# Optimization experiments

Hardware: AMD Instinct MI355X
Metric: run time of the kernel (lower is better)

## Reference

```python
import jax, jax.numpy as jnp
import numpy as np

C = 256
INTER = 32  # C // reduction_ratio(8)
B, H, W = 4, 64, 64


def setup_inputs() -> dict:
    key = jax.random.key(0)
    ks = jax.random.split(key, 8)
    x = jax.random.normal(ks[0], (B, C, H, W), dtype=jnp.float32)
    # 1x1 conv weights stored as [out, in] matrices + biases
    Wq = jax.random.normal(ks[1], (INTER, C), dtype=jnp.float32) * (1.0 / np.sqrt(C))
    bq = jnp.zeros((INTER,), dtype=jnp.float32)
    Wk = jax.random.normal(ks[2], (INTER, C), dtype=jnp.float32) * (1.0 / np.sqrt(C))
    bk = jnp.zeros((INTER,), dtype=jnp.float32)
    Wv = jax.random.normal(ks[3], (C, C), dtype=jnp.float32) * (1.0 / np.sqrt(C))
    bv = jnp.zeros((C,), dtype=jnp.float32)
    gamma = jnp.zeros((1,), dtype=jnp.float32)
    return {"x": x, "Wq": Wq, "bq": bq, "Wk": Wk, "bk": bk, "Wv": Wv, "bv": bv, "gamma": gamma}


def reference(x, Wq, bq, Wk, bk, Wv, bv, gamma):
    b, c, h, w = x.shape
    n = h * w
    xf = x.reshape(b, c, n)  # [B,C,N]
    # 1x1 convs == channel matmuls
    q = jnp.einsum('ic,bcn->bin', Wq, xf) + bq[None, :, None]  # [B,I,N]
    k = jnp.einsum('ic,bcn->bin', Wk, xf) + bk[None, :, None]  # [B,I,N]
    v = jnp.einsum('oc,bcn->bon', Wv, xf) + bv[None, :, None]  # [B,C,N]
    scale = INTER ** (-0.5)
    attn = jnp.einsum('bin,bim->bnm', q, k) * scale  # [B,N,N]
    attn = jax.nn.softmax(attn, axis=-1)
    out = jnp.einsum('bcm,bnm->bcn', v, attn)  # value @ attn^T
    out = out.reshape(b, c, h, w)
    return gamma[0] * out + x
```

## Files before the change

kernel.cpp:

```cpp
#include <hip/hip_runtime.h>
#include <hip/hip_bf16.h>
#include <cstddef>
#include <cstdint>

#define BB 4
#define CC 256
#define II 32
#define NN 4096

#define SCALE_Q 0.25505572751402893f

typedef __attribute__((ext_vector_type(8))) short bf16x8;
typedef __attribute__((ext_vector_type(16))) float f32x16;

static __device__ __forceinline__ int cvt_pk_bf16(float lo, float hi) {
  int d;
  asm("v_cvt_pk_bf16_f32 %0, %1, %2" : "=v"(d) : "v"(lo), "v"(hi));
  return d;
}
static __device__ __forceinline__ void perm32swap_i(int& a, int& b) {
  asm("v_permlane32_swap_b32 %0, %1" : "+v"(a), "+v"(b));
}
static __device__ __forceinline__ void perm32swap_f(float& a, float& b) {
  asm("v_permlane32_swap_b32 %0, %1" : "+v"(a), "+v"(b));
}
static __device__ __forceinline__ float max3f(float a, float b, float c) {
  float d;
  asm("v_max3_f32 %0, %1, %2, %3" : "=v"(d) : "v"(a), "v"(b), "v"(c));
  return d;
}
static __device__ __forceinline__ f32x16 zero16() {
  f32x16 z;
#pragma unroll
  for (int i = 0; i < 16; ++i) z[i] = 0.0f;
  return z;
}
static __device__ __forceinline__ bf16x8 pack8(float f0, float f1, float f2,
    float f3, float f4, float f5, float f6, float f7) {
  union { int w[4]; bf16x8 v8; } u;
  u.w[0] = cvt_pk_bf16(f0, f1);
  u.w[1] = cvt_pk_bf16(f2, f3);
  u.w[2] = cvt_pk_bf16(f4, f5);
  u.w[3] = cvt_pk_bf16(f6, f7);
  return u.v8;
}
static __device__ __forceinline__ ushort f2bfu(float f) {
  union { __hip_bfloat16 h; ushort u; } cv;
  cv.h = __float2bfloat16(f);
  return cv.u;
}
static __device__ __forceinline__ int pack4_fp8(float a, float b, float c, float d) {
  int r = __builtin_amdgcn_cvt_pk_fp8_f32(a, b, 0, false);
  r = __builtin_amdgcn_cvt_pk_fp8_f32(c, d, r, true);
  return r;
}
static __device__ __forceinline__ unsigned char f2fp8(float f) {
  return (unsigned char)(__builtin_amdgcn_cvt_pk_fp8_f32(f, f, 0, false) & 0xff);
}


__global__ __launch_bounds__(64, 3) void proj_mfma(
    const float* __restrict__ Wq, const float* __restrict__ bq,
    const float* __restrict__ Wk, const float* __restrict__ bk,
    const float* __restrict__ Wv, const float* __restrict__ bv,
    const float* __restrict__ x,
    ushort* __restrict__ qT, ushort* __restrict__ kT,
    unsigned char* __restrict__ vT8) {
  const int lane = threadIdx.x;
  const int l31 = lane & 31;
  const int h = lane >> 5;
  const int b = blockIdx.x;
  const int n0 = blockIdx.y * 32;
  const int og = blockIdx.z;

  const float* xb = x + (size_t)b * CC * NN + n0 + l31;
  const float* wr0 = (og == 0) ? (Wq + (size_t)l31 * CC)
                               : (Wv + (size_t)((og - 1) * 64 + l31) * CC);
  const float* wr1 = (og == 0) ? (Wk + (size_t)l31 * CC)
                               : (Wv + (size_t)((og - 1) * 64 + 32 + l31) * CC);

  f32x16 acc0 = zero16(), acc1 = zero16();
#pragma unroll 4
  for (int ks = 0; ks < 16; ++ks) {
    const int c = ks * 16 + h * 8;
    const float* xp = xb + (size_t)c * NN;
    bf16x8 xf = pack8(xp[0], xp[(size_t)1 * NN], xp[(size_t)2 * NN],
                      xp[(size_t)3 * NN], xp[(size_t)4 * NN], xp[(size_t)5 * NN],
                      xp[(size_t)6 * NN], xp[(size_t)7 * NN]);
    float4 wa = *(const float4*)(wr0 + c);
    float4 wb = *(const float4*)(wr0 + c + 4);
    bf16x8 wf0 = pack8(wa.x, wa.y, wa.z, wa.w, wb.x, wb.y, wb.z, wb.w);
    float4 wc = *(const float4*)(wr1 + c);
    float4 wd = *(const float4*)(wr1 + c + 4);
    bf16x8 wf1 = pack8(wc.x, wc.y, wc.z, wc.w, wd.x, wd.y, wd.z, wd.w);
    acc0 = __builtin_amdgcn_mfma_f32_32x32x16_bf16(wf0, xf, acc0, 0, 0, 0);
    acc1 = __builtin_amdgcn_mfma_f32_32x32x16_bf16(wf1, xf, acc1, 0, 0, 0);
  }

  if (og == 0) {
    ushort* qb = qT + (size_t)(b * 128 + (n0 >> 5)) * 1024;
    ushort* kb = kT + (size_t)(b * 128 + (n0 >> 5)) * 1024;
#pragma unroll
    for (int r = 0; r < 16; ++r) {
      const int i = (r & 3) + 8 * (r >> 2) + 4 * h;
      const size_t off = (size_t)(i >> 4) * 512 + ((i >> 3) & 1) * 256 + 8 * l31 + (i & 7);
      qb[off] = f2bfu((acc0[r] + bq[i]) * SCALE_Q);
      kb[off] = f2bfu(acc1[r] + bk[i]);
    }
  } else {
    const int n = n0 + l31;
    const size_t nbase = (size_t)b * (1 << 20) + (size_t)(n >> 4) * 4096 +
                         ((size_t)((n >> 3) & 1)) * 256 + (n & 7);
#pragma unroll
    for (int r = 0; r < 16; ++r) {
      const int rp = (r & 3) + 8 * (r >> 2) + 4 * h;
      const int c0 = (og - 1) * 64 + rp;
      const int c1 = c0 + 32;
      vT8[nbase + (size_t)(c0 >> 5) * 512 + (c0 & 31) * 8] = f2fp8(acc0[r] + bv[c0]);
      vT8[nbase + (size_t)(c1 >> 5) * 512 + (c1 & 31) * 8] = f2fp8(acc1[r] + bv[c1]);
    }
  }
}

__global__ __launch_bounds__(256, 2) void flash_mfma(
    const ushort* __restrict__ qT, const ushort* __restrict__ kT,
    const unsigned char* __restrict__ vT8, const float* __restrict__ x,
    const float* __restrict__ gamma, float* __restrict__ out) {
  __shared__ float smem[17152];
  float* B0 = smem;
  float* B1 = smem + 8448;
  float* ml = smem + 16896;
  float* ll = smem + 17024;

  const int tid = threadIdx.x;
  const int lane = tid & 63;
  const int w = tid >> 6;
  const int l31 = lane & 31;
  const int h = lane >> 5;

  const int wg = blockIdx.x;
  const int xcd = wg & 7;
  const int pos = wg >> 3;
  const int b = xcd >> 1;
  const int nt = ((xcd & 1) << 6) + pos;
  const int n0 = nt * 32;
  const int kbase = w * (NN / 4);

  const ushort* qb = qT + (size_t)(b * 128 + nt) * 1024 + lane * 8;
  const bf16x8 qf0 = *reinterpret_cast<const bf16x8*>(qb);
  const bf16x8 qf1 = *reinterpret_cast<const bf16x8*>(qb + 512);

  const ushort* ktb = kT + (size_t)b * 128 * 1024;
  const unsigned char* vtb = vT8 + (size_t)b * (1 << 20);

  f32x16 acc[8];
#pragma unroll
  for (int ct = 0; ct < 8; ++ct) acc[ct] = zero16();
  float m_run = -1e30f, l_run = 0.0f;

  for (int m0 = 0; m0 < NN / 4; m0 += 64) {
    const int kabs = kbase + m0;
    const ushort* kc = ktb + (size_t)(kabs >> 5) * 1024 + lane * 8;
    const bf16x8 kf00 = *reinterpret_cast<const bf16x8*>(kc);
    const bf16x8 kf01 = *reinterpret_cast<const bf16x8*>(kc + 512);
    const bf16x8 kf10 = *reinterpret_cast<const bf16x8*>(kc + 1024);
    const bf16x8 kf11 = *reinterpret_cast<const bf16x8*>(kc + 1536);
    f32x16 st0 = zero16(), st1 = zero16();
    st0 = __builtin_amdgcn_mfma_f32_32x32x16_bf16(kf00, qf0, st0, 0, 0, 0);
    st1 = __builtin_amdgcn_mfma_f32_32x32x16_bf16(kf10, qf0, st1, 0, 0, 0);
    st0 = __builtin_amdgcn_mfma_f32_32x32x16_bf16(kf01, qf1, st0, 0, 0, 0);
    st1 = __builtin_amdgcn_mfma_f32_32x32x16_bf16(kf11, qf1, st1, 0, 0, 0);

    float ma_ = max3f(st0[0], st0[1], st0[2]);
    float mb_ = max3f(st0[3], st0[4], st0[5]);
    float mc_ = max3f(st0[6], st0[7], st0[8]);
    float md_ = max3f(st0[9], st0[10], st0[11]);
    ma_ = max3f(st0[12], st0[13], ma_);
    mb_ = max3f(st0[14], st0[15], mb_);
    mc_ = max3f(st1[0], st1[1], mc_);
    md_ = max3f(st1[2], st1[3], md_);
    ma_ = max3f(st1[4], st1[5], ma_);
    mb_ = max3f(st1[6], st1[7], mb_);
    mc_ = max3f(st1[8], st1[9], mc_);
    md_ = max3f(st1[10], st1[11], md_);
    ma_ = max3f(st1[12], st1[13], ma_);
    mb_ = max3f(st1[14], st1[15], mb_);
    float mx = max3f(ma_, mb_, max3f(mc_, md_, -1e30f));
    float sw1 = mx, sw2 = mx;
    perm32swap_f(sw1, sw2);
    const float rowmax = fmaxf(sw1, sw2);

    if (__any(rowmax > m_run + 8.0f)) {
      const float mnew = fmaxf(m_run, rowmax);
      const float f = exp2f(m_run - mnew);
#pragma unroll
      for (int ct = 0; ct < 8; ++ct)
#pragma unroll
        for (int r = 0; r < 16; ++r) acc[ct][r] *= f;
      l_run *= f;
      m_run = mnew;
    }

#pragma unroll
    for (int r = 0; r < 16; ++r) st0[r] = exp2f(st0[r] - m_run);
#pragma unroll
    for (int r = 0; r < 16; ++r) st1[r] = exp2f(st1[r] - m_run);
    float s8[8];
#pragma unroll
    for (int r = 0; r < 8; ++r)
      s8[r] = (st0[r] + st0[r + 8]) + (st1[r] + st1[r + 8]);
    float ps = ((s8[0] + s8[1]) + (s8[2] + s8[3])) +
               ((s8[4] + s8[5]) + (s8[6] + s8[7]));
    float sa = ps, sb = ps;
    perm32swap_f(sa, sb);
    l_run += sa + sb;

    union LI { int w2[2]; long l; } pf0, pf1, pf2, pf3;
    {
      int A = pack4_fp8(st0[0], st0[1], st0[2], st0[3]);
      int B = pack4_fp8(st0[4], st0[5], st0[6], st0[7]);
      perm32swap_i(A, B);
      pf0.w2[0] = A; pf0.w2[1] = B;
    }
    {
      int A = pack4_fp8(st0[8], st0[9], st0[10], st0[11]);
      int B = pack4_fp8(st0[12], st0[13], st0[14], st0[15]);
      perm32swap_i(A, B);
      pf1.w2[0] = A; pf1.w2[1] = B;
    }
    {
      int A = pack4_fp8(st1[0], st1[1], st1[2], st1[3]);
      int B = pack4_fp8(st1[4], st1[5], st1[6], st1[7]);
      perm32swap_i(A, B);
      pf2.w2[0] = A; pf2.w2[1] = B;
    }
    {
      int A = pack4_fp8(st1[8], st1[9], st1[10], st1[11]);
      int B = pack4_fp8(st1[12], st1[13], st1[14], st1[15]);
      perm32swap_i(A, B);
      pf3.w2[0] = A; pf3.w2[1] = B;
    }
    const long pfl[4] = {pf0.l, pf1.l, pf2.l, pf3.l};

#pragma unroll
    for (int ksi = 0; ksi < 4; ++ksi) {
      const unsigned char* vc = vtb + (size_t)((kabs >> 4) + ksi) * 4096 + lane * 8;
#pragma unroll
      for (int ct = 0; ct < 8; ++ct) {
        const long vf = *reinterpret_cast<const long*>(vc + (size_t)ct * 512);
        acc[ct] = __builtin_amdgcn_mfma_f32_32x32x16_fp8_fp8(vf, pfl[ksi], acc[ct], 0, 0, 0);
      }
    }
  }

  if (h == 0) { ml[w * 32 + l31] = m_run; ll[w * 32 + l31] = l_run; }
  __syncthreads();
  const int q = tid & 31;
  const float m0_ = ml[q], m1_ = ml[32 + q], m2_ = ml[64 + q], m3_ = ml[96 + q];
  const float mt = fmaxf(fmaxf(m0_, m1_), fmaxf(m2_, m3_));
  const float f0 = exp2f(m0_ - mt), f1 = exp2f(m1_ - mt);
  const float f2 = exp2f(m2_ - mt), f3 = exp2f(m3_ - mt);
  const float lt = f0 * ll[q] + f1 * ll[32 + q] + f2 * ll[64 + q] + f3 * ll[96 + q];
  const float fmy = (w == 0) ? f0 : (w == 1) ? f1 : (w == 2) ? f2 : f3;

  if (w < 2) {
    float* Bd = (w == 0) ? B0 : B1;
#pragma unroll
    for (int ct = 0; ct < 8; ++ct)
#pragma unroll
      for (int r = 0; r < 16; ++r) {
        const int c = ct * 32 + (r & 3) + 8 * (r >> 2) + 4 * h;
        Bd[c * 33 + l31] = fmy * acc[ct][r];
      }
  }
  __syncthreads();
  if (w >= 2) {
    float* Bd = (w == 2) ? B0 : B1;
#pragma unroll
    for (int ct = 0; ct < 8; ++ct)
#pragma unroll
      for (int r = 0; r < 16; ++r) {
        const int c = ct * 32 + (r & 3) + 8 * (r >> 2) + 4 * h;
        Bd[c * 33 + l31] += fmy * acc[ct][r];
      }
  }
  __syncthreads();

  const float g = gamma[0];
  const float linv = 1.0f / lt;
#pragma unroll
  for (int rep = 0; rep < 32; ++rep) {
    const int flat = rep * 256 + tid;
    const int c = flat >> 5;
    const float o = B0[c * 33 + q] + B1[c * 33 + q];
    const size_t idx = ((size_t)b * CC + c) * NN + n0 + q;
    out[idx] = g * o * linv + x[idx];
  }
}

extern "C" void kernel_launch(void* const* d_in, const int* in_sizes, int n_in,
                              void* d_out, int out_size, void* d_ws, size_t ws_size,
                              hipStream_t stream) {
  const float* x = (const float*)d_in[0];
  const float* Wq = (const float*)d_in[1];
  const float* bq = (const float*)d_in[2];
  const float* Wk = (const float*)d_in[3];
  const float* bk = (const float*)d_in[4];
  const float* Wv = (const float*)d_in[5];
  const float* bv = (const float*)d_in[6];
  const float* gamma = (const float*)d_in[7];
  float* out = (float*)d_out;

  ushort* qT = (ushort*)d_ws;
  ushort* kT = qT + (size_t)BB * 128 * 1024;
  unsigned char* vT8 = (unsigned char*)(kT + (size_t)BB * 128 * 1024);

  proj_mfma<<<dim3(BB, NN / 32, 5), dim3(64), 0, stream>>>(
      Wq, bq, Wk, bk, Wv, bv, x, qT, kT, vT8);
  flash_mfma<<<dim3(512), dim3(256), 0, stream>>>(
      qT, kT, vT8, x, gamma, out);
}
```

Measured before the change: 80.22 us.

## Split flash attention over channel tiles with shared softmax via LDS

Replaces the key-split flash kernel (4 waves each owning a quarter of the keys and all 256 channels, merged at the end through LDS) with 8 waves per block that cooperate on each 256-key chunk. Each wave computes scores for 32 keys, a block-wide running max and sum are exchanged through LDS, and the fp8 probabilities are staged in a shared buffer so each wave accumulates one 32-channel output tile over all keys. This removes the large 8-tile accumulator register footprint and the final cross-wave reduction, allowing more waves per CU. The cost is two block barriers per iteration plus LDS traffic for the probabilities, and MFMA priority hints are added around the matrix ops.

```diff
diff --git a/kernel.cpp b/kernel.cpp
--- a/kernel.cpp
+++ b/kernel.cpp
@@ -17,9 +17,6 @@
   int d;
   asm("v_cvt_pk_bf16_f32 %0, %1, %2" : "=v"(d) : "v"(lo), "v"(hi));
   return d;
-}
-static __device__ __forceinline__ void perm32swap_i(int& a, int& b) {
-  asm("v_permlane32_swap_b32 %0, %1" : "+v"(a), "+v"(b));
 }
 static __device__ __forceinline__ void perm32swap_f(float& a, float& b) {
   asm("v_permlane32_swap_b32 %0, %1" : "+v"(a), "+v"(b));
@@ -122,29 +119,25 @@
   }
 }
 
-__global__ __launch_bounds__(256, 2) void flash_mfma(
+__global__ __launch_bounds__(512, 4) void flash_coop(
     const ushort* __restrict__ qT, const ushort* __restrict__ kT,
     const unsigned char* __restrict__ vT8, const float* __restrict__ x,
     const float* __restrict__ gamma, float* __restrict__ out) {
-  __shared__ float smem[17152];
-  float* B0 = smem;
-  float* B1 = smem + 8448;
-  float* ml = smem + 16896;
-  float* ll = smem + 17024;
+  __shared__ __align__(16) unsigned char pbuf[32 * 264];
+  __shared__ float mlds[264];
+  __shared__ float slds[264];
 
   const int tid = threadIdx.x;
   const int lane = tid & 63;
   const int w = tid >> 6;
-  const int l31 = lane & 31;
+  const int q = lane & 31;
   const int h = lane >> 5;
 
   const int wg = blockIdx.x;
   const int xcd = wg & 7;
-  const int pos = wg >> 3;
   const int b = xcd >> 1;
-  const int nt = ((xcd & 1) << 6) + pos;
+  const int nt = ((xcd & 1) << 6) + (wg >> 3);
   const int n0 = nt * 32;
-  const int kbase = w * (NN / 4);
 
   const ushort* qb = qT + (size_t)(b * 128 + nt) * 1024 + lane * 8;
   const bf16x8 qf0 = *reinterpret_cast<const bf16x8*>(qb);
@@ -153,148 +146,87 @@
   const ushort* ktb = kT + (size_t)b * 128 * 1024;
   const unsigned char* vtb = vT8 + (size_t)b * (1 << 20);
 
-  f32x16 acc[8];
-#pragma unroll
-  for (int ct = 0; ct < 8; ++ct) acc[ct] = zero16();
+  f32x16 acc = zero16();
   float m_run = -1e30f, l_run = 0.0f;
 
-  for (int m0 = 0; m0 < NN / 4; m0 += 64) {
-    const int kabs = kbase + m0;
-    const ushort* kc = ktb + (size_t)(kabs >> 5) * 1024 + lane * 8;
-    const bf16x8 kf00 = *reinterpret_cast<const bf16x8*>(kc);
-    const bf16x8 kf01 = *reinterpret_cast<const bf16x8*>(kc + 512);
-    const bf16x8 kf10 = *reinterpret_cast<const bf16x8*>(kc + 1024);
-    const bf16x8 kf11 = *reinterpret_cast<const bf16x8*>(kc + 1536);
-    f32x16 st0 = zero16(), st1 = zero16();
-    st0 = __builtin_amdgcn_mfma_f32_32x32x16_bf16(kf00, qf0, st0, 0, 0, 0);
-    st1 = __builtin_amdgcn_mfma_f32_32x32x16_bf16(kf10, qf0, st1, 0, 0, 0);
-    st0 = __builtin_amdgcn_mfma_f32_32x32x16_bf16(kf01, qf1, st0, 0, 0, 0);
-    st1 = __builtin_amdgcn_mfma_f32_32x32x16_bf16(kf11, qf1, st1, 0, 0, 0);
-
-    float ma_ = max3f(st0[0], st0[1], st0[2]);
-    float mb_ = max3f(st0[3], st0[4], st0[5]);
-    float mc_ = max3f(st0[6], st0[7], st0[8]);
-    float md_ = max3f(st0[9], st0[10], st0[11]);
-    ma_ = max3f(st0[12], st0[13], ma_);
-    mb_ = max3f(st0[14], st0[15], mb_);
-    mc_ = max3f(st1[0], st1[1], mc_);
-    md_ = max3f(st1[2], st1[3], md_);
-    ma_ = max3f(st1[4], st1[5], ma_);
-    mb_ = max3f(st1[6], st1[7], mb_);
-    mc_ = max3f(st1[8], st1[9], mc_);
-    md_ = max3f(st1[10], st1[11], md_);
-    ma_ = max3f(st1[12], st1[13], ma_);
-    mb_ = max3f(st1[14], st1[15], mb_);
-    float mx = max3f(ma_, mb_, max3f(mc_, md_, -1e30f));
+  for (int it = 0; it < 16; ++it) {
+    const ushort* kc = ktb + (size_t)(it * 8 + w) * 1024 + lane * 8;
+    const bf16x8 kf0 = *reinterpret_cast<const bf16x8*>(kc);
+    const bf16x8 kf1 = *reinterpret_cast<const bf16x8*>(kc + 512);
+    f32x16 st = zero16();
+    __builtin_amdgcn_s_setprio(1);
+    st = __builtin_amdgcn_mfma_f32_32x32x16_bf16(kf0, qf0, st, 0, 0, 0);
+    st = __builtin_amdgcn_mfma_f32_32x32x16_bf16(kf1, qf1, st, 0, 0, 0);
+    __builtin_amdgcn_s_setprio(0);
+
+    float m0 = max3f(st[0], st[1], st[2]);
+    float m1 = max3f(st[3], st[4], st[5]);
+    float m2 = max3f(st[6], st[7], st[8]);
+    float m3 = max3f(st[9], st[10], st[11]);
+    m0 = max3f(st[12], st[13], m0);
+    m1 = max3f(st[14], st[15], m1);
+    float mx = max3f(m0, m1, fmaxf(m2, m3));
     float sw1 = mx, sw2 = mx;
     perm32swap_f(sw1, sw2);
-    const float rowmax = fmaxf(sw1, sw2);
-
-    if (__any(rowmax > m_run + 8.0f)) {
-      const float mnew = fmaxf(m_run, rowmax);
+    const float wmax = fmaxf(sw1, sw2);
+    if (lane < 32) mlds[w * 33 + q] = wmax;
+    __syncthreads();
+
+    float tmax = mlds[q];
+#pragma unroll
+    for (int i = 1; i < 8; ++i) tmax = fmaxf(tmax, mlds[i * 33 + q]);
+
+    if (__any(tmax > m_run + 8.0f)) {
+      const float mnew = fmaxf(m_run, tmax);
       const float f = exp2f(m_run - mnew);
 #pragma unroll
-      for (int ct = 0; ct < 8; ++ct)
-#pragma unroll
-        for (int r = 0; r < 16; ++r) acc[ct][r] *= f;
+      for (int r = 0; r < 16; ++r) acc[r] *= f;
       l_run *= f;
       m_run = mnew;
     }
 
 #pragma unroll
-    for (int r = 0; r < 16; ++r) st0[r] = exp2f(st0[r] - m_run);
-#pragma unroll
-    for (int r = 0; r < 16; ++r) st1[r] = exp2f(st1[r] - m_run);
-    float s8[8];
-#pragma unroll
-    for (int r = 0; r < 8; ++r)
-      s8[r] = (st0[r] + st0[r + 8]) + (st1[r] + st1[r + 8]);
-    float ps = ((s8[0] + s8[1]) + (s8[2] + s8[3])) +
-               ((s8[4] + s8[5]) + (s8[6] + s8[7]));
-    float sa = ps, sb = ps;
-    perm32swap_f(sa, sb);
-    l_run += sa + sb;
-
-    union LI { int w2[2]; long l; } pf0, pf1, pf2, pf3;
-    {
-      int A = pack4_fp8(st0[0], st0[1], st0[2], st0[3]);
-      int B = pack4_fp8(st0[4], st0[5], st0[6], st0[7]);
-      perm32swap_i(A, B);
-      pf0.w2[0] = A; pf0.w2[1] = B;
-    }
-    {
-      int A = pack4_fp8(st0[8], st0[9], st0[10], st0[11]);
-      int B = pack4_fp8(st0[12], st0[13], st0[14], st0[15]);
-      perm32swap_i(A, B);
-      pf1.w2[0] = A; pf1.w2[1] = B;
-    }
-    {
-      int A = pack4_fp8(st1[0], st1[1], st1[2], st1[3]);
-      int B = pack4_fp8(st1[4], st1[5], st1[6], st1[7]);
-      perm32swap_i(A, B);
-      pf2.w2[0] = A; pf2.w2[1] = B;
-    }
-    {
-      int A = pack4_fp8(st1[8], st1[9], st1[10], st1[11]);
-      int B = pack4_fp8(st1[12], st1[13], st1[14], st1[15]);
-      perm32swap_i(A, B);
-      pf3.w2[0] = A; pf3.w2[1] = B;
-    }
-    const long pfl[4] = {pf0.l, pf1.l, pf2.l, pf3.l};
-
-#pragma unroll
-    for (int ksi = 0; ksi < 4; ++ksi) {
-      const unsigned char* vc = vtb + (size_t)((kabs >> 4) + ksi) * 4096 + lane * 8;
-#pragma unroll
-      for (int ct = 0; ct < 8; ++ct) {
-        const long vf = *reinterpret_cast<const long*>(vc + (size_t)ct * 512);
-        acc[ct] = __builtin_amdgcn_mfma_f32_32x32x16_fp8_fp8(vf, pfl[ksi], acc[ct], 0, 0, 0);
-      }
-    }
-  }
-
-  if (h == 0) { ml[w * 32 + l31] = m_run; ll[w * 32 + l31] = l_run; }
-  __syncthreads();
-  const int q = tid & 31;
-  const float m0_ = ml[q], m1_ = ml[32 + q], m2_ = ml[64 + q], m3_ = ml[96 + q];
-  const float mt = fmaxf(fmaxf(m0_, m1_), fmaxf(m2_, m3_));
-  const float f0 = exp2f(m0_ - mt), f1 = exp2f(m1_ - mt);
-  const float f2 = exp2f(m2_ - mt), f3 = exp2f(m3_ - mt);
-  const float lt = f0 * ll[q] + f1 * ll[32 + q] + f2 * ll[64 + q] + f3 * ll[96 + q];
-  const float fmy = (w == 0) ? f0 : (w == 1) ? f1 : (w == 2) ? f2 : f3;
-
-  if (w < 2) {
-    float* Bd = (w == 0) ? B0 : B1;
-#pragma unroll
-    for (int ct = 0; ct < 8; ++ct)
-#pragma unroll
-      for (int r = 0; r < 16; ++r) {
-        const int c = ct * 32 + (r & 3) + 8 * (r >> 2) + 4 * h;
-        Bd[c * 33 + l31] = fmy * acc[ct][r];
-      }
-  }
-  __syncthreads();
-  if (w >= 2) {
-    float* Bd = (w == 2) ? B0 : B1;
-#pragma unroll
-    for (int ct = 0; ct < 8; ++ct)
-#pragma unroll
-      for (int r = 0; r < 16; ++r) {
-        const int c = ct * 32 + (r & 3) + 8 * (r >> 2) + 4 * h;
-        Bd[c * 33 + l31] += fmy * acc[ct][r];
-      }
-  }
-  __syncthreads();
+    for (int r = 0; r < 16; ++r) st[r] = exp2f(st[r] - m_run);
+    float s0 = ((st[0] + st[1]) + (st[2] + st[3])) +
+               ((st[4] + st[5]) + (st[6] + st[7]));
+    float s1 = ((st[8] + st[9]) + (st[10] + st[11])) +
+               ((st[12] + st[13]) + (st[14] + st[15]));
+    float pssum = s0 + s1;
+    float pa = pssum, pb = pssum;
+    perm32swap_f(pa, pb);
+    pssum = pa + pb;
+    if (lane < 32) slds[w * 33 + q] = pssum;
+
+#pragma unroll
+    for (int rg = 0; rg < 4; ++rg) {
+      const int pk = pack4_fp8(st[rg * 4], st[rg * 4 + 1], st[rg * 4 + 2], st[rg * 4 + 3]);
+      *reinterpret_cast<int*>(&pbuf[q * 264 + w * 32 + rg * 8 + h * 4]) = pk;
+    }
+    __syncthreads();
+
+    float tsum = slds[q];
+#pragma unroll
+    for (int i = 1; i < 8; ++i) tsum += slds[i * 33 + q];
+    l_run += tsum;
+
+    const unsigned char* vc = vtb + (size_t)(it * 16) * 4096 + w * 512 + lane * 8;
+    __builtin_amdgcn_s_setprio(1);
+#pragma unroll
+    for (int kt = 0; kt < 16; ++kt) {
+      const long vf = *reinterpret_cast<const long*>(vc + (size_t)kt * 4096);
+      const long pfr = *reinterpret_cast<const long*>(&pbuf[q * 264 + kt * 16 + h * 8]);
+      acc = __builtin_amdgcn_mfma_f32_32x32x16_fp8_fp8(vf, pfr, acc, 0, 0, 0);
+    }
+    __builtin_amdgcn_s_setprio(0);
+  }
 
   const float g = gamma[0];
-  const float linv = 1.0f / lt;
-#pragma unroll
-  for (int rep = 0; rep < 32; ++rep) {
-    const int flat = rep * 256 + tid;
-    const int c = flat >> 5;
-    const float o = B0[c * 33 + q] + B1[c * 33 + q];
+  const float linv = 1.0f / l_run;
+#pragma unroll
+  for (int r = 0; r < 16; ++r) {
+    const int c = w * 32 + (r & 3) + 8 * (r >> 2) + 4 * h;
     const size_t idx = ((size_t)b * CC + c) * NN + n0 + q;
-    out[idx] = g * o * linv + x[idx];
+    out[idx] = g * acc[r] * linv + x[idx];
   }
 }
 
@@ -317,6 +249,6 @@
 
   proj_mfma<<<dim3(BB, NN / 32, 5), dim3(64), 0, stream>>>(
       Wq, bq, Wk, bk, Wv, bv, x, qT, kT, vT8);
-  flash_mfma<<<dim3(512), dim3(256), 0, stream>>>(
+  flash_coop<<<dim3(512), dim3(512), 0, stream>>>(
       qT, kT, vT8, x, gamma, out);
 }
```

Measured after the change: 84.57 us. +5.4%, slower.
